# Optimization experiments

Hardware: AMD Instinct MI355X
Metric: run time of the kernel (lower is better)

## Reference

```python
import jax, jax.numpy as jnp
import numpy as np
import math

B, N, D = 4, 16384, 256
M, H = 64, 8
HD = D // H

def setup_inputs() -> dict:
    key = jax.random.key(0)
    ks = jax.random.split(key, 5)
    s = 1.0 / math.sqrt(D)
    return {
        "x": jax.random.normal(ks[0], (B, N, D), dtype=jnp.float32),
        "Ws": jax.random.normal(ks[1], (M, D), dtype=jnp.float32) * s,
        "bs": jnp.zeros((M,), dtype=jnp.float32),
        "Wqkv": jax.random.normal(ks[2], (3 * D, D), dtype=jnp.float32) * s,
        "Wo": jax.random.normal(ks[3], (D, D), dtype=jnp.float32) * s,
        "bo": jnp.zeros((D,), dtype=jnp.float32),
    }

def reference(x, Ws, bs, Wqkv, Wo, bo):
    # slice weights: softmax over N (dim=1), matching the torch code exactly
    logits = jnp.einsum('bnd,md->bnm', x, Ws) + bs          # [B,N,M]
    weights = jax.nn.softmax(logits, axis=1)                # softmax over N
    # pooling: tokens[b,m,d] = sum_n w[b,n,m] * x[b,n,d]
    tokens = jnp.einsum('bnm,bnd->bmd', weights, x)         # [B,M,D]
    # qkv projection (no bias)
    qkv = jnp.einsum('bmd,ed->bme', tokens, Wqkv)           # [B,M,3D]
    qkv = qkv.reshape(B, M, 3, H, HD)
    q = qkv[:, :, 0].transpose(0, 2, 1, 3)                  # [B,H,M,HD]
    k = qkv[:, :, 1].transpose(0, 2, 1, 3)
    v = qkv[:, :, 2].transpose(0, 2, 1, 3)
    scale = 1.0 / math.sqrt(HD)
    attn = jax.nn.softmax(jnp.einsum('bhmd,bhkd->bhmk', q, k) * scale, axis=-1)
    token_out = jnp.einsum('bhmk,bhkd->bhmd', attn, v)      # [B,H,M,HD]
    token_out = token_out.transpose(0, 2, 1, 3).reshape(B, M, D)
    token_out = jnp.einsum('bmd,ed->bme', token_out, Wo) + bo
    # unpooling: out[b,n,d] = sum_m w[b,n,m] * token_out[b,m,d]
    out = jnp.einsum('bnm,bmd->bnd', weights, token_out)    # [B,N,D]
    return out
```

## Files before the change

kernel.cpp:

```cpp
#include <hip/hip_runtime.h>
#include <math.h>

constexpr int B = 4;
constexpr int N = 16384;
constexpr int D = 256;
constexpr int M = 64;
constexpr int H = 8;

typedef __attribute__((ext_vector_type(8))) short short8;
typedef __attribute__((ext_vector_type(4))) float floatx4;

__device__ __forceinline__ float4 ld4(const float* p) {
  return *reinterpret_cast<const float4*>(p);
}
__device__ __forceinline__ unsigned short f2bf(float f) {
  unsigned u = __float_as_uint(f);
  unsigned r = (u + 0x7fffu + ((u >> 16) & 1u)) >> 16;
  return (unsigned short)r;
}

__global__ __launch_bounds__(256) void k0_prep(
    const float* __restrict__ Ws, const float* __restrict__ Wqkv,
    const float* __restrict__ Wo, unsigned short* __restrict__ WsB,
    unsigned short* __restrict__ WqkvB, unsigned short* __restrict__ WoB,
    float* __restrict__ denom, float* __restrict__ tokens,
    float* __restrict__ tokO) {
  const int g = blockIdx.x * 256 + threadIdx.x;
  if (g < 32768) {
    *reinterpret_cast<float2*>(&tokens[g * 2]) = make_float2(0.f, 0.f);
    *reinterpret_cast<float2*>(&tokO[g * 2]) = make_float2(0.f, 0.f);
  }
  if (g < 128)
    *reinterpret_cast<float2*>(&denom[g * 2]) = make_float2(0.f, 0.f);
  const float* src;
  unsigned short* dst;
  int off;
  if (g < 2048) {
    src = Ws; dst = WsB; off = g;
  } else if (g < 26624) {
    src = Wqkv; dst = WqkvB; off = g - 2048;
  } else {
    src = Wo; dst = WoB; off = g - 26624;
  }
  const float4 a = ld4(&src[(size_t)off * 8]);
  const float4 c = ld4(&src[(size_t)off * 8 + 4]);
  unsigned d0 = (unsigned)f2bf(a.x) | ((unsigned)f2bf(a.y) << 16);
  unsigned d1 = (unsigned)f2bf(a.z) | ((unsigned)f2bf(a.w) << 16);
  unsigned d2 = (unsigned)f2bf(c.x) | ((unsigned)f2bf(c.y) << 16);
  unsigned d3 = (unsigned)f2bf(c.z) | ((unsigned)f2bf(c.w) << 16);
  *reinterpret_cast<uint4*>(&dst[(size_t)off * 8]) = make_uint4(d0, d1, d2, d3);
}

__global__ __launch_bounds__(512, 4) void k1_fused(
    const float* __restrict__ x, const unsigned short* __restrict__ WsB,
    const float* __restrict__ bs, unsigned short* __restrict__ En,
    float* __restrict__ denom) {
  __shared__ unsigned short Wt[64][264];
  __shared__ float red[64];
  const int b = blockIdx.y;
  const int n0 = blockIdx.x * 128;
  const int tid = threadIdx.x;
  const int w = tid >> 6, l = tid & 63;
  const int l15 = l & 15;
  const int q8 = (l >> 4) * 8;
  const int ar = w * 16 + l15;

  float4 fx[16];
  const float* xrow = &x[((size_t)(b * N + n0 + ar)) * D];
#pragma unroll
  for (int ks = 0; ks < 8; ++ks) {
    fx[2 * ks] = ld4(&xrow[ks * 32 + q8]);
    fx[2 * ks + 1] = ld4(&xrow[ks * 32 + q8 + 4]);
  }
#pragma unroll
  for (int p = 0; p < 4; ++p) {
    const int u = p * 512 + tid;
    const int row = u >> 5;
    const int c = (u & 31) * 8;
    *reinterpret_cast<short8*>(&Wt[row][c]) =
        *reinterpret_cast<const short8*>(&WsB[(size_t)row * 256 + c]);
  }
  if (tid < 64) red[tid] = 0.0f;

  short8 afr[8];
#pragma unroll
  for (int ks = 0; ks < 8; ++ks) {
    const float4 a0 = fx[2 * ks], a1 = fx[2 * ks + 1];
    short8 t;
    t[0] = (short)f2bf(a0.x); t[1] = (short)f2bf(a0.y);
    t[2] = (short)f2bf(a0.z); t[3] = (short)f2bf(a0.w);
    t[4] = (short)f2bf(a1.x); t[5] = (short)f2bf(a1.y);
    t[6] = (short)f2bf(a1.z); t[7] = (short)f2bf(a1.w);
    afr[ks] = t;
  }
  __syncthreads();

  floatx4 acc[4] = {{0.f, 0.f, 0.f, 0.f},
                    {0.f, 0.f, 0.f, 0.f},
                    {0.f, 0.f, 0.f, 0.f},
                    {0.f, 0.f, 0.f, 0.f}};
#pragma unroll
  for (int ks = 0; ks < 8; ++ks) {
#pragma unroll
    for (int mt = 0; mt < 4; ++mt) {
      short8 bf = *reinterpret_cast<short8*>(&Wt[mt * 16 + l15][ks * 32 + q8]);
      acc[mt] = __builtin_amdgcn_mfma_f32_16x16x32_bf16(afr[ks], bf, acc[mt], 0, 0, 0);
    }
  }

#pragma unroll
  for (int mt = 0; mt < 4; ++mt) {
    const int m = mt * 16 + l15;
    const float bsm = bs[m];
    float s = 0.0f;
#pragma unroll
    for (int r = 0; r < 4; ++r) {
      const int n = w * 16 + (l >> 4) * 4 + r;
      const float e = expf(acc[mt][r] + bsm);
      s += e;
      En[((size_t)(b * N + n0 + n)) * M + m] = f2bf(e);
    }
    atomicAdd(&red[m], s);
  }
  __syncthreads();
  if (tid < 64) atomicAdd(&denom[b * M + tid], red[tid]);
}

__global__ __launch_bounds__(256) void k2_pool(
    const unsigned short* __restrict__ En, const float* __restrict__ x,
    float* __restrict__ tokens) {
  __shared__ unsigned short Ens[64][70];
  __shared__ unsigned short XsT[64][72];
  const int dt = blockIdx.x, nc = blockIdx.y, b = blockIdx.z;
  const int d0 = dt * 64;
  const int tid = threadIdx.x;
  const int w = tid >> 6, l = tid & 63;
  const int l15 = l & 15;
  const int q8 = (l >> 4) * 8;
  floatx4 acc[4] = {{0.f, 0.f, 0.f, 0.f},
                    {0.f, 0.f, 0.f, 0.f},
                    {0.f, 0.f, 0.f, 0.f},
                    {0.f, 0.f, 0.f, 0.f}};
  for (int kc = 0; kc < 4; ++kc) {
    const int nb = nc * 256 + kc * 64;
    __syncthreads();
#pragma unroll
    for (int p = 0; p < 2; ++p) {
      const int u = p * 256 + tid;
      const int n = u >> 3;
      const int c8 = (u & 7) * 8;
      short8 v = *reinterpret_cast<const short8*>(
          &En[((size_t)(b * N + nb + n)) * M + c8]);
      uint4 uv = *reinterpret_cast<uint4*>(&v);
      unsigned* dp = reinterpret_cast<unsigned*>(&Ens[n][c8]);
      dp[0] = uv.x; dp[1] = uv.y; dp[2] = uv.z; dp[3] = uv.w;
    }
    {
      const int n = tid >> 2;
      const int c16 = (tid & 3) * 16;
      const float* xp = &x[((size_t)(b * N + nb + n)) * D + d0 + c16];
#pragma unroll
      for (int q = 0; q < 4; ++q) {
        float4 v = ld4(xp + q * 4);
        XsT[c16 + q * 4 + 0][n] = f2bf(v.x);
        XsT[c16 + q * 4 + 1][n] = f2bf(v.y);
        XsT[c16 + q * 4 + 2][n] = f2bf(v.z);
        XsT[c16 + q * 4 + 3][n] = f2bf(v.w);
      }
    }
    __syncthreads();
#pragma unroll
    for (int ks = 0; ks < 2; ++ks) {
      const int nf = ks * 32 + q8;
      short8 a;
#pragma unroll
      for (int j = 0; j < 8; ++j) a[j] = (short)Ens[nf + j][w * 16 + l15];
#pragma unroll
      for (int dtile = 0; dtile < 4; ++dtile) {
        short8 bf = *reinterpret_cast<short8*>(&XsT[dtile * 16 + l15][nf]);
        acc[dtile] =
            __builtin_amdgcn_mfma_f32_16x16x32_bf16(a, bf, acc[dtile], 0, 0, 0);
      }
    }
  }
#pragma unroll
  for (int dtile = 0; dtile < 4; ++dtile)
#pragma unroll
    for (int r = 0; r < 4; ++r) {
      const int m = w * 16 + (l >> 4) * 4 + r;
      const int d = d0 + dtile * 16 + (l & 15);
      atomicAdd(&tokens[((size_t)(b * M + m)) * D + d], acc[dtile][r]);
    }
}

__global__ __launch_bounds__(256) void k_fa(
    const float* __restrict__ tokens, const unsigned short* __restrict__ WqkvB,
    const unsigned short* __restrict__ WoB, const float* __restrict__ denom,
    float* __restrict__ tokO) {
  __shared__ __align__(16) char smem[84480];
  unsigned short* const At = reinterpret_cast<unsigned short*>(smem);
  unsigned short* const Wq = reinterpret_cast<unsigned short*>(smem + 33792);
  float* const qt = reinterpret_cast<float*>(smem);
  float* const kt = reinterpret_cast<float*>(smem + 8704);
  float* const vv = reinterpret_cast<float*>(smem + 17408);
  float* const P  = reinterpret_cast<float*>(smem + 26624);
  float* const ao = reinterpret_cast<float*>(smem + 44032);
  const int b = blockIdx.x >> 3;
  const int h = blockIdx.x & 7;
  const int tid = threadIdx.x;
  const int w = tid >> 6, l = tid & 63;
  const int l15 = l & 15;
  const int q8 = (l >> 4) * 8;
  const int r4 = (l >> 4) * 4;

#pragma unroll
  for (int p = 0; p < 16; ++p) {
    const int i = p * 256 + tid;
    const int row = i >> 6;
    const int c4 = (i & 63) * 4;
    float4 av = ld4(&tokens[((size_t)(b * M + row)) * D + c4]);
    unsigned a0 = (unsigned)f2bf(av.x) | ((unsigned)f2bf(av.y) << 16);
    unsigned a1 = (unsigned)f2bf(av.z) | ((unsigned)f2bf(av.w) << 16);
    *reinterpret_cast<uint2*>(&At[row * 264 + c4]) = make_uint2(a0, a1);
  }
#pragma unroll
  for (int p = 0; p < 12; ++p) {
    const int u = p * 256 + tid;
    const int row = u >> 5;
    const int c = (u & 31) * 8;
    const int eg = (row < 32) ? (h * 32 + row)
                 : (row < 64) ? (256 + h * 32 + row - 32)
                              : (512 + h * 32 + row - 64);
    *reinterpret_cast<short8*>(&Wq[row * 264 + c]) =
        *reinterpret_cast<const short8*>(&WqkvB[(size_t)eg * 256 + c]);
  }
  float rcp4[4];
#pragma unroll
  for (int r = 0; r < 4; ++r)
    rcp4[r] = 1.0f / denom[b * M + w * 16 + r4 + r];
  __syncthreads();

  floatx4 acc[6] = {{0.f, 0.f, 0.f, 0.f}, {0.f, 0.f, 0.f, 0.f},
                    {0.f, 0.f, 0.f, 0.f}, {0.f, 0.f, 0.f, 0.f},
                    {0.f, 0.f, 0.f, 0.f}, {0.f, 0.f, 0.f, 0.f}};
  const int arow = w * 16 + l15;
#pragma unroll
  for (int ks = 0; ks < 8; ++ks) {
    short8 a = *reinterpret_cast<short8*>(&At[arow * 264 + ks * 32 + q8]);
#pragma unroll
    for (int et = 0; et < 6; ++et) {
      short8 bf = *reinterpret_cast<short8*>(&Wq[(et * 16 + l15) * 264 + ks * 32 + q8]);
      acc[et] = __builtin_amdgcn_mfma_f32_16x16x32_bf16(a, bf, acc[et], 0, 0, 0);
    }
  }
  short8 wof[4];
#pragma unroll
  for (int dt4 = 0; dt4 < 4; ++dt4)
    wof[dt4] = *reinterpret_cast<const short8*>(
        &WoB[(size_t)(w * 64 + dt4 * 16 + l15) * 256 + h * 32 + q8]);
  __syncthreads();

#pragma unroll
  for (int r = 0; r < 4; ++r) {
    const int m = w * 16 + r4 + r;
    const float rc = rcp4[r];
#pragma unroll
    for (int et = 0; et < 6; ++et) {
      const float val = acc[et][r] * rc;
      const int c = (et & 1) * 16 + l15;
      if (et < 2) qt[c * 68 + m] = val;
      else if (et < 4) kt[c * 68 + m] = val;
      else vv[m * 36 + c] = val;
    }
  }
  __syncthreads();

  {
    const int tm4 = (tid & 15) * 4;
    const int tn4 = (tid >> 4) * 4;
    float sacc[4][4] = {};
    for (int k = 0; k < 32; ++k) {
      float4 a4 = ld4(&qt[k * 68 + tn4]);
      float4 b4 = ld4(&kt[k * 68 + tm4]);
#pragma unroll
      for (int i = 0; i < 4; ++i) {
        const float av = (i == 0) ? a4.x : (i == 1) ? a4.y : (i == 2) ? a4.z : a4.w;
        sacc[i][0] = fmaf(av, b4.x, sacc[i][0]);
        sacc[i][1] = fmaf(av, b4.y, sacc[i][1]);
        sacc[i][2] = fmaf(av, b4.z, sacc[i][2]);
        sacc[i][3] = fmaf(av, b4.w, sacc[i][3]);
      }
    }
    const float scale = 0.17677669529663687f;
#pragma unroll
    for (int i = 0; i < 4; ++i)
      *reinterpret_cast<float4*>(&P[(tn4 + i) * 68 + tm4]) =
          make_float4(sacc[i][0] * scale, sacc[i][1] * scale,
                      sacc[i][2] * scale, sacc[i][3] * scale);
  }
  __syncthreads();
  if (tid < 64) {
    float mx = -1e30f;
    for (int j = 0; j < 64; ++j) mx = fmaxf(mx, P[tid * 68 + j]);
    float s = 0.0f;
    for (int j = 0; j < 64; ++j) {
      const float e = expf(P[tid * 68 + j] - mx);
      P[tid * 68 + j] = e;
      s += e;
    }
    const float r = 1.0f / s;
    for (int j = 0; j < 64; ++j) P[tid * 68 + j] *= r;
  }
  __syncthreads();
  if (tid < 128) {
    const int i0 = (tid >> 3) * 4;
    const int c0 = (tid & 7) * 4;
    float o[4][4] = {};
    for (int j = 0; j < 64; ++j) {
      float4 v4 = ld4(&vv[j * 36 + c0]);
#pragma unroll
      for (int ii = 0; ii < 4; ++ii) {
        const float p = P[(i0 + ii) * 68 + j];
        o[ii][0] = fmaf(p, v4.x, o[ii][0]);
        o[ii][1] = fmaf(p, v4.y, o[ii][1]);
        o[ii][2] = fmaf(p, v4.z, o[ii][2]);
        o[ii][3] = fmaf(p, v4.w, o[ii][3]);
      }
    }
#pragma unroll
    for (int ii = 0; ii < 4; ++ii)
#pragma unroll
      for (int jj = 0; jj < 4; ++jj) ao[(i0 + ii) * 36 + c0 + jj] = o[ii][jj];
  }
  __syncthreads();

  floatx4 acc2[4][4] = {{{0.f, 0.f, 0.f, 0.f}, {0.f, 0.f, 0.f, 0.f},
                         {0.f, 0.f, 0.f, 0.f}, {0.f, 0.f, 0.f, 0.f}},
                        {{0.f, 0.f, 0.f, 0.f}, {0.f, 0.f, 0.f, 0.f},
                         {0.f, 0.f, 0.f, 0.f}, {0.f, 0.f, 0.f, 0.f}},
                        {{0.f, 0.f, 0.f, 0.f}, {0.f, 0.f, 0.f, 0.f},
                         {0.f, 0.f, 0.f, 0.f}, {0.f, 0.f, 0.f, 0.f}},
                        {{0.f, 0.f, 0.f, 0.f}, {0.f, 0.f, 0.f, 0.f},
                         {0.f, 0.f, 0.f, 0.f}, {0.f, 0.f, 0.f, 0.f}}};
#pragma unroll
  for (int mt = 0; mt < 4; ++mt) {
    short8 af;
#pragma unroll
    for (int j = 0; j < 8; ++j)
      af[j] = (short)f2bf(ao[(mt * 16 + l15) * 36 + q8 + j]);
#pragma unroll
    for (int dt4 = 0; dt4 < 4; ++dt4)
      acc2[mt][dt4] =
          __builtin_amdgcn_mfma_f32_16x16x32_bf16(af, wof[dt4], acc2[mt][dt4], 0, 0, 0);
  }
#pragma unroll
  for (int mt = 0; mt < 4; ++mt)
#pragma unroll
    for (int dt4 = 0; dt4 < 4; ++dt4)
#pragma unroll
      for (int r = 0; r < 4; ++r) {
        const int m = mt * 16 + r4 + r;
        const int d = w * 64 + dt4 * 16 + l15;
        atomicAdd(&tokO[((size_t)(b * M + m)) * D + d], acc2[mt][dt4][r]);
      }
}

__global__ __launch_bounds__(512, 4) void k6_unpool(
    const unsigned short* __restrict__ En, const float* __restrict__ tokO,
    const float* __restrict__ denom, const float* __restrict__ bo,
    float* __restrict__ out) {
  __shared__ unsigned short EnS[128][72];
  __shared__ unsigned short TpS[64][72];
  const int dt = blockIdx.x, nt = blockIdx.y, b = blockIdx.z;
  const int n0 = nt * 128, d0 = dt * 64;
  const int tid = threadIdx.x;
  const int w = tid >> 6, l = tid & 63;
  const int l15 = l & 15;
  const int q8 = (l >> 4) * 8;
#pragma unroll
  for (int p = 0; p < 2; ++p) {
    const int g = p * 512 + tid;
    const int row = g >> 3;
    const int c8 = (g & 7) * 8;
    *reinterpret_cast<short8*>(&EnS[row][c8]) =
        *reinterpret_cast<const short8*>(
            &En[((size_t)(b * N + n0 + row)) * M + c8]);
  }
  {
    const int m = tid >> 3;
    const int c8 = (tid & 7) * 8;
    const float rc = 1.0f / denom[b * M + m];
    const float* tp = &tokO[((size_t)(b * M + m)) * D + d0 + c8];
    float4 v0 = ld4(tp);
    float4 v1 = ld4(tp + 4);
    float4 bb0 = ld4(&bo[d0 + c8]);
    float4 bb1 = ld4(&bo[d0 + c8 + 4]);
    TpS[c8 + 0][m] = f2bf((v0.x + bb0.x) * rc);
    TpS[c8 + 1][m] = f2bf((v0.y + bb0.y) * rc);
    TpS[c8 + 2][m] = f2bf((v0.z + bb0.z) * rc);
    TpS[c8 + 3][m] = f2bf((v0.w + bb0.w) * rc);
    TpS[c8 + 4][m] = f2bf((v1.x + bb1.x) * rc);
    TpS[c8 + 5][m] = f2bf((v1.y + bb1.y) * rc);
    TpS[c8 + 6][m] = f2bf((v1.z + bb1.z) * rc);
    TpS[c8 + 7][m] = f2bf((v1.w + bb1.w) * rc);
  }
  __syncthreads();
  floatx4 acc[4] = {{0.f, 0.f, 0.f, 0.f},
                    {0.f, 0.f, 0.f, 0.f},
                    {0.f, 0.f, 0.f, 0.f},
                    {0.f, 0.f, 0.f, 0.f}};
  const int arow = w * 16 + l15;
#pragma unroll
  for (int ks = 0; ks < 2; ++ks) {
    short8 a = *reinterpret_cast<short8*>(&EnS[arow][ks * 32 + q8]);
#pragma unroll
    for (int dtile = 0; dtile < 4; ++dtile) {
      short8 bf = *reinterpret_cast<short8*>(
          &TpS[dtile * 16 + l15][ks * 32 + q8]);
      acc[dtile] =
          __builtin_amdgcn_mfma_f32_16x16x32_bf16(a, bf, acc[dtile], 0, 0, 0);
    }
  }
#pragma unroll
  for (int dtile = 0; dtile < 4; ++dtile)
#pragma unroll
    for (int r = 0; r < 4; ++r) {
      const int n = n0 + w * 16 + (l >> 4) * 4 + r;
      const int d = d0 + dtile * 16 + l15;
      out[((size_t)(b * N + n)) * D + d] = acc[dtile][r];
    }
}

extern "C" void kernel_launch(void* const* d_in, const int* in_sizes, int n_in,
                              void* d_out, int out_size, void* d_ws,
                              size_t ws_size, hipStream_t stream) {
  const float* x = (const float*)d_in[0];
  const float* Ws = (const float*)d_in[1];
  const float* bs = (const float*)d_in[2];
  const float* Wqkv = (const float*)d_in[3];
  const float* Wo = (const float*)d_in[4];
  const float* bo = (const float*)d_in[5];
  float* out = (float*)d_out;

  char* p = (char*)d_ws;
  unsigned short* En = (unsigned short*)p;    p += (size_t)B * N * M * 2;
  float* denom = (float*)p;                   p += (size_t)B * M * 4;
  float* tokens = (float*)p;                  p += (size_t)B * M * D * 4;
  float* tokO = (float*)p;                    p += (size_t)B * M * D * 4;
  unsigned short* WsB = (unsigned short*)p;   p += (size_t)M * D * 2;
  unsigned short* WqkvB = (unsigned short*)p; p += (size_t)3 * D * D * 2;
  unsigned short* WoB = (unsigned short*)p;   p += (size_t)D * D * 2;

  k0_prep<<<dim3(136), 256, 0, stream>>>(Ws, Wqkv, Wo, WsB, WqkvB, WoB,
                                         denom, tokens, tokO);
  k1_fused<<<dim3(N / 128, B), 512, 0, stream>>>(x, WsB, bs, En, denom);
  k2_pool<<<dim3(D / 64, N / 256, B), 256, 0, stream>>>(En, x, tokens);
  k_fa<<<dim3(B * H), 256, 0, stream>>>(tokens, WqkvB, WoB, denom, tokO);
  k6_unpool<<<dim3(D / 64, N / 128, B), 512, 0, stream>>>(En, tokO, denom, bo,
                                                          out);
}
```

Measured before the change: 174.6 us.

## Fuse slice-logit exp kernel with pooling GEMM to reuse x tile on-chip

Merges the logit/exp kernel and the pooling kernel into one. Each block now processes 128 tokens in two 64-row passes, keeping the bf16 x fragments and the exp weights in shared memory and feeding them straight into the pooling MFMAs. This removes the second full read of x and the En read-back in the pool kernel, plus one launch. In exchange, per-block register pressure rises (16 accumulator tiles), blocks shrink to 256 threads, and each block now issues 64x256 atomic adds to tokens, so global atomic traffic grows.

```diff
diff --git a/kernel.cpp b/kernel.cpp
--- a/kernel.cpp
+++ b/kernel.cpp
@@ -51,145 +51,125 @@
   *reinterpret_cast<uint4*>(&dst[(size_t)off * 8]) = make_uint4(d0, d1, d2, d3);
 }
 
-__global__ __launch_bounds__(512, 4) void k1_fused(
+__global__ __launch_bounds__(256, 2) void k12_fused(
     const float* __restrict__ x, const unsigned short* __restrict__ WsB,
     const float* __restrict__ bs, unsigned short* __restrict__ En,
-    float* __restrict__ denom) {
+    float* __restrict__ denom, float* __restrict__ tokens) {
   __shared__ unsigned short Wt[64][264];
+  __shared__ unsigned short EsT[64][70];
+  __shared__ unsigned short XsT[256][70];
   __shared__ float red[64];
   const int b = blockIdx.y;
-  const int n0 = blockIdx.x * 128;
+  const int nb0 = blockIdx.x * 128;
   const int tid = threadIdx.x;
   const int w = tid >> 6, l = tid & 63;
   const int l15 = l & 15;
   const int q8 = (l >> 4) * 8;
+  const int r4 = (l >> 4) * 4;
   const int ar = w * 16 + l15;
 
-  float4 fx[16];
-  const float* xrow = &x[((size_t)(b * N + n0 + ar)) * D];
-#pragma unroll
-  for (int ks = 0; ks < 8; ++ks) {
-    fx[2 * ks] = ld4(&xrow[ks * 32 + q8]);
-    fx[2 * ks + 1] = ld4(&xrow[ks * 32 + q8 + 4]);
-  }
-#pragma unroll
-  for (int p = 0; p < 4; ++p) {
-    const int u = p * 512 + tid;
+#pragma unroll
+  for (int p = 0; p < 8; ++p) {
+    const int u = p * 256 + tid;
     const int row = u >> 5;
     const int c = (u & 31) * 8;
     *reinterpret_cast<short8*>(&Wt[row][c]) =
         *reinterpret_cast<const short8*>(&WsB[(size_t)row * 256 + c]);
   }
   if (tid < 64) red[tid] = 0.0f;
-
-  short8 afr[8];
-#pragma unroll
-  for (int ks = 0; ks < 8; ++ks) {
-    const float4 a0 = fx[2 * ks], a1 = fx[2 * ks + 1];
-    short8 t;
-    t[0] = (short)f2bf(a0.x); t[1] = (short)f2bf(a0.y);
-    t[2] = (short)f2bf(a0.z); t[3] = (short)f2bf(a0.w);
-    t[4] = (short)f2bf(a1.x); t[5] = (short)f2bf(a1.y);
-    t[6] = (short)f2bf(a1.z); t[7] = (short)f2bf(a1.w);
-    afr[ks] = t;
-  }
-  __syncthreads();
-
-  floatx4 acc[4] = {{0.f, 0.f, 0.f, 0.f},
-                    {0.f, 0.f, 0.f, 0.f},
-                    {0.f, 0.f, 0.f, 0.f},
-                    {0.f, 0.f, 0.f, 0.f}};
-#pragma unroll
-  for (int ks = 0; ks < 8; ++ks) {
+  __syncthreads();
+
+  floatx4 acc2[16];
+#pragma unroll
+  for (int i = 0; i < 16; ++i) acc2[i] = {0.f, 0.f, 0.f, 0.f};
+
+  for (int t = 0; t < 2; ++t) {
+    const int n0 = nb0 + t * 64;
+    float4 fx[16];
+    const float* xrow = &x[((size_t)(b * N + n0 + ar)) * D];
+#pragma unroll
+    for (int ks = 0; ks < 8; ++ks) {
+      fx[2 * ks] = ld4(&xrow[ks * 32 + q8]);
+      fx[2 * ks + 1] = ld4(&xrow[ks * 32 + q8 + 4]);
+    }
+    short8 afr[8];
+#pragma unroll
+    for (int ks = 0; ks < 8; ++ks) {
+      const float4 a0 = fx[2 * ks], a1 = fx[2 * ks + 1];
+      short8 tt;
+      tt[0] = (short)f2bf(a0.x); tt[1] = (short)f2bf(a0.y);
+      tt[2] = (short)f2bf(a0.z); tt[3] = (short)f2bf(a0.w);
+      tt[4] = (short)f2bf(a1.x); tt[5] = (short)f2bf(a1.y);
+      tt[6] = (short)f2bf(a1.z); tt[7] = (short)f2bf(a1.w);
+      afr[ks] = tt;
+    }
+
+    floatx4 acc[4] = {{0.f, 0.f, 0.f, 0.f},
+                      {0.f, 0.f, 0.f, 0.f},
+                      {0.f, 0.f, 0.f, 0.f},
+                      {0.f, 0.f, 0.f, 0.f}};
+#pragma unroll
+    for (int ks = 0; ks < 8; ++ks) {
+#pragma unroll
+      for (int mt = 0; mt < 4; ++mt) {
+        short8 bf = *reinterpret_cast<short8*>(&Wt[mt * 16 + l15][ks * 32 + q8]);
+        acc[mt] =
+            __builtin_amdgcn_mfma_f32_16x16x32_bf16(afr[ks], bf, acc[mt], 0, 0, 0);
+      }
+    }
+
+    unsigned short ebf[16];
 #pragma unroll
     for (int mt = 0; mt < 4; ++mt) {
-      short8 bf = *reinterpret_cast<short8*>(&Wt[mt * 16 + l15][ks * 32 + q8]);
-      acc[mt] = __builtin_amdgcn_mfma_f32_16x16x32_bf16(afr[ks], bf, acc[mt], 0, 0, 0);
-    }
-  }
-
-#pragma unroll
-  for (int mt = 0; mt < 4; ++mt) {
-    const int m = mt * 16 + l15;
-    const float bsm = bs[m];
-    float s = 0.0f;
-#pragma unroll
-    for (int r = 0; r < 4; ++r) {
-      const int n = w * 16 + (l >> 4) * 4 + r;
-      const float e = expf(acc[mt][r] + bsm);
-      s += e;
-      En[((size_t)(b * N + n0 + n)) * M + m] = f2bf(e);
-    }
-    atomicAdd(&red[m], s);
-  }
-  __syncthreads();
-  if (tid < 64) atomicAdd(&denom[b * M + tid], red[tid]);
-}
-
-__global__ __launch_bounds__(256) void k2_pool(
-    const unsigned short* __restrict__ En, const float* __restrict__ x,
-    float* __restrict__ tokens) {
-  __shared__ unsigned short Ens[64][70];
-  __shared__ unsigned short XsT[64][72];
-  const int dt = blockIdx.x, nc = blockIdx.y, b = blockIdx.z;
-  const int d0 = dt * 64;
-  const int tid = threadIdx.x;
-  const int w = tid >> 6, l = tid & 63;
-  const int l15 = l & 15;
-  const int q8 = (l >> 4) * 8;
-  floatx4 acc[4] = {{0.f, 0.f, 0.f, 0.f},
-                    {0.f, 0.f, 0.f, 0.f},
-                    {0.f, 0.f, 0.f, 0.f},
-                    {0.f, 0.f, 0.f, 0.f}};
-  for (int kc = 0; kc < 4; ++kc) {
-    const int nb = nc * 256 + kc * 64;
+      const int m = mt * 16 + l15;
+      const float bsm = bs[m];
+      float s = 0.0f;
+#pragma unroll
+      for (int r = 0; r < 4; ++r) {
+        const int n = w * 16 + r4 + r;
+        const float e = expf(acc[mt][r] + bsm);
+        s += e;
+        const unsigned short eb = f2bf(e);
+        ebf[mt * 4 + r] = eb;
+        En[((size_t)(b * N + n0 + n)) * M + m] = eb;
+      }
+      atomicAdd(&red[m], s);
+    }
+
     __syncthreads();
 #pragma unroll
-    for (int p = 0; p < 2; ++p) {
-      const int u = p * 256 + tid;
-      const int n = u >> 3;
-      const int c8 = (u & 7) * 8;
-      short8 v = *reinterpret_cast<const short8*>(
-          &En[((size_t)(b * N + nb + n)) * M + c8]);
-      uint4 uv = *reinterpret_cast<uint4*>(&v);
-      unsigned* dp = reinterpret_cast<unsigned*>(&Ens[n][c8]);
-      dp[0] = uv.x; dp[1] = uv.y; dp[2] = uv.z; dp[3] = uv.w;
-    }
-    {
-      const int n = tid >> 2;
-      const int c16 = (tid & 3) * 16;
-      const float* xp = &x[((size_t)(b * N + nb + n)) * D + d0 + c16];
-#pragma unroll
-      for (int q = 0; q < 4; ++q) {
-        float4 v = ld4(xp + q * 4);
-        XsT[c16 + q * 4 + 0][n] = f2bf(v.x);
-        XsT[c16 + q * 4 + 1][n] = f2bf(v.y);
-        XsT[c16 + q * 4 + 2][n] = f2bf(v.z);
-        XsT[c16 + q * 4 + 3][n] = f2bf(v.w);
-      }
-    }
+    for (int ks = 0; ks < 8; ++ks)
+#pragma unroll
+      for (int j = 0; j < 8; ++j)
+        XsT[ks * 32 + q8 + j][ar] = (unsigned short)afr[ks][j];
+#pragma unroll
+    for (int mt = 0; mt < 4; ++mt)
+#pragma unroll
+      for (int r = 0; r < 4; ++r)
+        EsT[mt * 16 + l15][w * 16 + r4 + r] = ebf[mt * 4 + r];
     __syncthreads();
+
 #pragma unroll
     for (int ks = 0; ks < 2; ++ks) {
       const int nf = ks * 32 + q8;
-      short8 a;
-#pragma unroll
-      for (int j = 0; j < 8; ++j) a[j] = (short)Ens[nf + j][w * 16 + l15];
-#pragma unroll
-      for (int dtile = 0; dtile < 4; ++dtile) {
-        short8 bf = *reinterpret_cast<short8*>(&XsT[dtile * 16 + l15][nf]);
-        acc[dtile] =
-            __builtin_amdgcn_mfma_f32_16x16x32_bf16(a, bf, acc[dtile], 0, 0, 0);
-      }
-    }
-  }
-#pragma unroll
-  for (int dtile = 0; dtile < 4; ++dtile)
+      short8 a = *reinterpret_cast<short8*>(&EsT[w * 16 + l15][nf]);
+#pragma unroll
+      for (int dt4 = 0; dt4 < 16; ++dt4) {
+        short8 bf = *reinterpret_cast<short8*>(&XsT[dt4 * 16 + l15][nf]);
+        acc2[dt4] =
+            __builtin_amdgcn_mfma_f32_16x16x32_bf16(a, bf, acc2[dt4], 0, 0, 0);
+      }
+    }
+  }
+
+  if (tid < 64) atomicAdd(&denom[b * M + tid], red[tid]);
+#pragma unroll
+  for (int dt4 = 0; dt4 < 16; ++dt4)
 #pragma unroll
     for (int r = 0; r < 4; ++r) {
-      const int m = w * 16 + (l >> 4) * 4 + r;
-      const int d = d0 + dtile * 16 + (l & 15);
-      atomicAdd(&tokens[((size_t)(b * M + m)) * D + d], acc[dtile][r]);
+      const int m = w * 16 + r4 + r;
+      const int d = dt4 * 16 + l15;
+      atomicAdd(&tokens[((size_t)(b * M + m)) * D + d], acc2[dt4][r]);
     }
 }
 
@@ -453,8 +433,8 @@
 
   k0_prep<<<dim3(136), 256, 0, stream>>>(Ws, Wqkv, Wo, WsB, WqkvB, WoB,
                                          denom, tokens, tokO);
-  k1_fused<<<dim3(N / 128, B), 512, 0, stream>>>(x, WsB, bs, En, denom);
-  k2_pool<<<dim3(D / 64, N / 256, B), 256, 0, stream>>>(En, x, tokens);
+  k12_fused<<<dim3(N / 128, B), 256, 0, stream>>>(x, WsB, bs, En, denom,
+                                                  tokens);
   k_fa<<<dim3(B * H), 256, 0, stream>>>(tokens, WqkvB, WoB, denom, tokO);
   k6_unpool<<<dim3(D / 64, N / 128, B), 512, 0, stream>>>(En, tokO, denom, bo,
                                                           out);
```

New measurement: 176.3 us. Within noise of the previous version (+1.0%).

## Replace global atomics with per-slot partials and a reduce kernel; drop prep kernel

Applied to the files above, without the earlier changes.

Pooling and denominator accumulation now write per-chunk partial sums to workspace slots. A new reduce kernel sums them, zeroes tokO, converts tokens to bf16 and precomputes reciprocal denominators. This removes float atomics and the separate prep/zero kernel. Weight conversion to bf16 moves inline into the consuming kernels, expf becomes __expf, and unpool blocks cover 256 rows in two passes. The cost is extra global traffic for the partial buffers (about 16 MB written then read) plus one more launch.

```diff
diff --git a/kernel.cpp b/kernel.cpp
--- a/kernel.cpp
+++ b/kernel.cpp
@@ -6,6 +6,8 @@
 constexpr int D = 256;
 constexpr int M = 64;
 constexpr int H = 8;
+constexpr int NSLOT_T = 64;
+constexpr int NSLOT_D = 128;
 
 typedef __attribute__((ext_vector_type(8))) short short8;
 typedef __attribute__((ext_vector_type(4))) float floatx4;
@@ -18,43 +20,18 @@
   unsigned r = (u + 0x7fffu + ((u >> 16) & 1u)) >> 16;
   return (unsigned short)r;
 }
-
-__global__ __launch_bounds__(256) void k0_prep(
-    const float* __restrict__ Ws, const float* __restrict__ Wqkv,
-    const float* __restrict__ Wo, unsigned short* __restrict__ WsB,
-    unsigned short* __restrict__ WqkvB, unsigned short* __restrict__ WoB,
-    float* __restrict__ denom, float* __restrict__ tokens,
-    float* __restrict__ tokO) {
-  const int g = blockIdx.x * 256 + threadIdx.x;
-  if (g < 32768) {
-    *reinterpret_cast<float2*>(&tokens[g * 2]) = make_float2(0.f, 0.f);
-    *reinterpret_cast<float2*>(&tokO[g * 2]) = make_float2(0.f, 0.f);
-  }
-  if (g < 128)
-    *reinterpret_cast<float2*>(&denom[g * 2]) = make_float2(0.f, 0.f);
-  const float* src;
-  unsigned short* dst;
-  int off;
-  if (g < 2048) {
-    src = Ws; dst = WsB; off = g;
-  } else if (g < 26624) {
-    src = Wqkv; dst = WqkvB; off = g - 2048;
-  } else {
-    src = Wo; dst = WoB; off = g - 26624;
-  }
-  const float4 a = ld4(&src[(size_t)off * 8]);
-  const float4 c = ld4(&src[(size_t)off * 8 + 4]);
+__device__ __forceinline__ uint2 pack8(float4 a, float4 b, unsigned* hi) {
   unsigned d0 = (unsigned)f2bf(a.x) | ((unsigned)f2bf(a.y) << 16);
   unsigned d1 = (unsigned)f2bf(a.z) | ((unsigned)f2bf(a.w) << 16);
-  unsigned d2 = (unsigned)f2bf(c.x) | ((unsigned)f2bf(c.y) << 16);
-  unsigned d3 = (unsigned)f2bf(c.z) | ((unsigned)f2bf(c.w) << 16);
-  *reinterpret_cast<uint4*>(&dst[(size_t)off * 8]) = make_uint4(d0, d1, d2, d3);
-}
-
-__global__ __launch_bounds__(512, 4) void k1_fused(
-    const float* __restrict__ x, const unsigned short* __restrict__ WsB,
+  hi[0] = (unsigned)f2bf(b.x) | ((unsigned)f2bf(b.y) << 16);
+  hi[1] = (unsigned)f2bf(b.z) | ((unsigned)f2bf(b.w) << 16);
+  return make_uint2(d0, d1);
+}
+
+__global__ __launch_bounds__(512, 4) void k1_logits(
+    const float* __restrict__ x, const float* __restrict__ Ws,
     const float* __restrict__ bs, unsigned short* __restrict__ En,
-    float* __restrict__ denom) {
+    float* __restrict__ denomP) {
   __shared__ unsigned short Wt[64][264];
   __shared__ float red[64];
   const int b = blockIdx.y;
@@ -63,6 +40,7 @@
   const int w = tid >> 6, l = tid & 63;
   const int l15 = l & 15;
   const int q8 = (l >> 4) * 8;
+  const int r4 = (l >> 4) * 4;
   const int ar = w * 16 + l15;
 
   float4 fx[16];
@@ -73,12 +51,17 @@
     fx[2 * ks + 1] = ld4(&xrow[ks * 32 + q8 + 4]);
   }
 #pragma unroll
-  for (int p = 0; p < 4; ++p) {
-    const int u = p * 512 + tid;
-    const int row = u >> 5;
-    const int c = (u & 31) * 8;
-    *reinterpret_cast<short8*>(&Wt[row][c]) =
-        *reinterpret_cast<const short8*>(&WsB[(size_t)row * 256 + c]);
+  for (int p = 0; p < 2; ++p) {
+    const int i = p * 512 + tid;
+    const int row = i >> 4;
+    const int c16 = (i & 15) * 16;
+    const float* wp = &Ws[(size_t)row * 256 + c16];
+    float4 v0 = ld4(wp), v1 = ld4(wp + 4), v2 = ld4(wp + 8), v3 = ld4(wp + 12);
+    unsigned hi[2];
+    uint2 lo = pack8(v0, v1, hi);
+    *reinterpret_cast<uint4*>(&Wt[row][c16]) = make_uint4(lo.x, lo.y, hi[0], hi[1]);
+    lo = pack8(v2, v3, hi);
+    *reinterpret_cast<uint4*>(&Wt[row][c16 + 8]) = make_uint4(lo.x, lo.y, hi[0], hi[1]);
   }
   if (tid < 64) red[tid] = 0.0f;
 
@@ -115,20 +98,21 @@
     float s = 0.0f;
 #pragma unroll
     for (int r = 0; r < 4; ++r) {
-      const int n = w * 16 + (l >> 4) * 4 + r;
-      const float e = expf(acc[mt][r] + bsm);
+      const int n = w * 16 + r4 + r;
+      const float e = __expf(acc[mt][r] + bsm);
       s += e;
       En[((size_t)(b * N + n0 + n)) * M + m] = f2bf(e);
     }
     atomicAdd(&red[m], s);
   }
   __syncthreads();
-  if (tid < 64) atomicAdd(&denom[b * M + tid], red[tid]);
+  if (tid < 64)
+    denomP[((size_t)(b * NSLOT_D) + blockIdx.x) * M + tid] = red[tid];
 }
 
 __global__ __launch_bounds__(256) void k2_pool(
     const unsigned short* __restrict__ En, const float* __restrict__ x,
-    float* __restrict__ tokens) {
+    float* __restrict__ tokensP) {
   __shared__ unsigned short Ens[64][70];
   __shared__ unsigned short XsT[64][72];
   const int dt = blockIdx.x, nc = blockIdx.y, b = blockIdx.z;
@@ -183,19 +167,46 @@
       }
     }
   }
+  float* op = tokensP + ((size_t)(b * NSLOT_T + nc) * M) * D;
 #pragma unroll
   for (int dtile = 0; dtile < 4; ++dtile)
 #pragma unroll
     for (int r = 0; r < 4; ++r) {
       const int m = w * 16 + (l >> 4) * 4 + r;
-      const int d = d0 + dtile * 16 + (l & 15);
-      atomicAdd(&tokens[((size_t)(b * M + m)) * D + d], acc[dtile][r]);
-    }
+      op[(size_t)m * D + d0 + dtile * 16 + l15] = acc[dtile][r];
+    }
+}
+
+__global__ __launch_bounds__(256) void k2r_reduce(
+    const float* __restrict__ tokensP, const float* __restrict__ denomP,
+    unsigned short* __restrict__ tokensB, float* __restrict__ rdenom,
+    float* __restrict__ tokO) {
+  const int b = blockIdx.x >> 6;
+  const int m = blockIdx.x & 63;
+  const int d = threadIdx.x;
+  tokO[(size_t)blockIdx.x * 256 + d] = 0.0f;
+  const float* base = tokensP + ((size_t)(b * NSLOT_T) * M + m) * D + d;
+  float s0 = 0.f, s1 = 0.f, s2 = 0.f, s3 = 0.f;
+#pragma unroll 4
+  for (int s = 0; s < NSLOT_T; s += 4) {
+    s0 += base[(size_t)(s + 0) * M * D];
+    s1 += base[(size_t)(s + 1) * M * D];
+    s2 += base[(size_t)(s + 2) * M * D];
+    s3 += base[(size_t)(s + 3) * M * D];
+  }
+  tokensB[((size_t)(b * M) + m) * D + d] = f2bf((s0 + s1) + (s2 + s3));
+  if (d < 64) {
+    float v = denomP[((size_t)(b * NSLOT_D) + d) * M + m] +
+              denomP[((size_t)(b * NSLOT_D) + 64 + d) * M + m];
+#pragma unroll
+    for (int off = 32; off > 0; off >>= 1) v += __shfl_down(v, off);
+    if (d == 0) rdenom[b * M + m] = 1.0f / v;
+  }
 }
 
 __global__ __launch_bounds__(256) void k_fa(
-    const float* __restrict__ tokens, const unsigned short* __restrict__ WqkvB,
-    const unsigned short* __restrict__ WoB, const float* __restrict__ denom,
+    const unsigned short* __restrict__ tokensB, const float* __restrict__ Wqkv,
+    const float* __restrict__ Wo, const float* __restrict__ rdenom,
     float* __restrict__ tokO) {
   __shared__ __align__(16) char smem[84480];
   unsigned short* const At = reinterpret_cast<unsigned short*>(smem);
@@ -214,30 +225,35 @@
   const int r4 = (l >> 4) * 4;
 
 #pragma unroll
-  for (int p = 0; p < 16; ++p) {
-    const int i = p * 256 + tid;
-    const int row = i >> 6;
-    const int c4 = (i & 63) * 4;
-    float4 av = ld4(&tokens[((size_t)(b * M + row)) * D + c4]);
-    unsigned a0 = (unsigned)f2bf(av.x) | ((unsigned)f2bf(av.y) << 16);
-    unsigned a1 = (unsigned)f2bf(av.z) | ((unsigned)f2bf(av.w) << 16);
-    *reinterpret_cast<uint2*>(&At[row * 264 + c4]) = make_uint2(a0, a1);
-  }
-#pragma unroll
-  for (int p = 0; p < 12; ++p) {
+  for (int p = 0; p < 8; ++p) {
     const int u = p * 256 + tid;
     const int row = u >> 5;
     const int c = (u & 31) * 8;
+    *reinterpret_cast<short8*>(&At[row * 264 + c]) =
+        *reinterpret_cast<const short8*>(&tokensB[((size_t)(b * M + row)) * 256 + c]);
+  }
+#pragma unroll
+  for (int p = 0; p < 6; ++p) {
+    const int u = p * 256 + tid;
+    const int row = u >> 4;
+    const int c16 = (u & 15) * 16;
     const int eg = (row < 32) ? (h * 32 + row)
                  : (row < 64) ? (256 + h * 32 + row - 32)
                               : (512 + h * 32 + row - 64);
-    *reinterpret_cast<short8*>(&Wq[row * 264 + c]) =
-        *reinterpret_cast<const short8*>(&WqkvB[(size_t)eg * 256 + c]);
+    const float* wp = &Wqkv[(size_t)eg * 256 + c16];
+    float4 v0 = ld4(wp), v1 = ld4(wp + 4), v2 = ld4(wp + 8), v3 = ld4(wp + 12);
+    unsigned hi[2];
+    uint2 lo = pack8(v0, v1, hi);
+    *reinterpret_cast<uint4*>(&Wq[row * 264 + c16]) =
+        make_uint4(lo.x, lo.y, hi[0], hi[1]);
+    lo = pack8(v2, v3, hi);
+    *reinterpret_cast<uint4*>(&Wq[row * 264 + c16 + 8]) =
+        make_uint4(lo.x, lo.y, hi[0], hi[1]);
   }
   float rcp4[4];
 #pragma unroll
   for (int r = 0; r < 4; ++r)
-    rcp4[r] = 1.0f / denom[b * M + w * 16 + r4 + r];
+    rcp4[r] = rdenom[b * M + w * 16 + r4 + r];
   __syncthreads();
 
   floatx4 acc[6] = {{0.f, 0.f, 0.f, 0.f}, {0.f, 0.f, 0.f, 0.f},
@@ -255,9 +271,16 @@
   }
   short8 wof[4];
 #pragma unroll
-  for (int dt4 = 0; dt4 < 4; ++dt4)
-    wof[dt4] = *reinterpret_cast<const short8*>(
-        &WoB[(size_t)(w * 64 + dt4 * 16 + l15) * 256 + h * 32 + q8]);
+  for (int dt4 = 0; dt4 < 4; ++dt4) {
+    const float* wp = &Wo[(size_t)(w * 64 + dt4 * 16 + l15) * 256 + h * 32 + q8];
+    float4 v0 = ld4(wp), v1 = ld4(wp + 4);
+    short8 tt;
+    tt[0] = (short)f2bf(v0.x); tt[1] = (short)f2bf(v0.y);
+    tt[2] = (short)f2bf(v0.z); tt[3] = (short)f2bf(v0.w);
+    tt[4] = (short)f2bf(v1.x); tt[5] = (short)f2bf(v1.y);
+    tt[6] = (short)f2bf(v1.z); tt[7] = (short)f2bf(v1.w);
+    wof[dt4] = tt;
+  }
   __syncthreads();
 
 #pragma unroll
@@ -367,18 +390,18 @@
 
 __global__ __launch_bounds__(512, 4) void k6_unpool(
     const unsigned short* __restrict__ En, const float* __restrict__ tokO,
-    const float* __restrict__ denom, const float* __restrict__ bo,
+    const float* __restrict__ rdenom, const float* __restrict__ bo,
     float* __restrict__ out) {
-  __shared__ unsigned short EnS[128][72];
+  __shared__ unsigned short EnS[256][72];
   __shared__ unsigned short TpS[64][72];
   const int dt = blockIdx.x, nt = blockIdx.y, b = blockIdx.z;
-  const int n0 = nt * 128, d0 = dt * 64;
+  const int n0 = nt * 256, d0 = dt * 64;
   const int tid = threadIdx.x;
   const int w = tid >> 6, l = tid & 63;
   const int l15 = l & 15;
   const int q8 = (l >> 4) * 8;
 #pragma unroll
-  for (int p = 0; p < 2; ++p) {
+  for (int p = 0; p < 4; ++p) {
     const int g = p * 512 + tid;
     const int row = g >> 3;
     const int c8 = (g & 7) * 8;
@@ -389,7 +412,7 @@
   {
     const int m = tid >> 3;
     const int c8 = (tid & 7) * 8;
-    const float rc = 1.0f / denom[b * M + m];
+    const float rc = rdenom[b * M + m];
     const float* tp = &tokO[((size_t)(b * M + m)) * D + d0 + c8];
     float4 v0 = ld4(tp);
     float4 v1 = ld4(tp + 4);
@@ -405,30 +428,33 @@
     TpS[c8 + 7][m] = f2bf((v1.w + bb1.w) * rc);
   }
   __syncthreads();
-  floatx4 acc[4] = {{0.f, 0.f, 0.f, 0.f},
-                    {0.f, 0.f, 0.f, 0.f},
-                    {0.f, 0.f, 0.f, 0.f},
-                    {0.f, 0.f, 0.f, 0.f}};
-  const int arow = w * 16 + l15;
-#pragma unroll
-  for (int ks = 0; ks < 2; ++ks) {
-    short8 a = *reinterpret_cast<short8*>(&EnS[arow][ks * 32 + q8]);
-#pragma unroll
-    for (int dtile = 0; dtile < 4; ++dtile) {
-      short8 bf = *reinterpret_cast<short8*>(
-          &TpS[dtile * 16 + l15][ks * 32 + q8]);
-      acc[dtile] =
-          __builtin_amdgcn_mfma_f32_16x16x32_bf16(a, bf, acc[dtile], 0, 0, 0);
-    }
-  }
-#pragma unroll
-  for (int dtile = 0; dtile < 4; ++dtile)
-#pragma unroll
-    for (int r = 0; r < 4; ++r) {
-      const int n = n0 + w * 16 + (l >> 4) * 4 + r;
-      const int d = d0 + dtile * 16 + l15;
-      out[((size_t)(b * N + n)) * D + d] = acc[dtile][r];
-    }
+#pragma unroll
+  for (int pass = 0; pass < 2; ++pass) {
+    const int arow = pass * 128 + w * 16 + l15;
+    floatx4 acc[4] = {{0.f, 0.f, 0.f, 0.f},
+                      {0.f, 0.f, 0.f, 0.f},
+                      {0.f, 0.f, 0.f, 0.f},
+                      {0.f, 0.f, 0.f, 0.f}};
+#pragma unroll
+    for (int ks = 0; ks < 2; ++ks) {
+      short8 a = *reinterpret_cast<short8*>(&EnS[arow][ks * 32 + q8]);
+#pragma unroll
+      for (int dtile = 0; dtile < 4; ++dtile) {
+        short8 bf = *reinterpret_cast<short8*>(
+            &TpS[dtile * 16 + l15][ks * 32 + q8]);
+        acc[dtile] =
+            __builtin_amdgcn_mfma_f32_16x16x32_bf16(a, bf, acc[dtile], 0, 0, 0);
+      }
+    }
+#pragma unroll
+    for (int dtile = 0; dtile < 4; ++dtile)
+#pragma unroll
+      for (int r = 0; r < 4; ++r) {
+        const int n = n0 + pass * 128 + w * 16 + (l >> 4) * 4 + r;
+        const int d = d0 + dtile * 16 + l15;
+        out[((size_t)(b * N + n)) * D + d] = acc[dtile][r];
+      }
+  }
 }
 
 extern "C" void kernel_launch(void* const* d_in, const int* in_sizes, int n_in,
@@ -443,19 +469,18 @@
   float* out = (float*)d_out;
 
   char* p = (char*)d_ws;
-  unsigned short* En = (unsigned short*)p;    p += (size_t)B * N * M * 2;
-  float* denom = (float*)p;                   p += (size_t)B * M * 4;
-  float* tokens = (float*)p;                  p += (size_t)B * M * D * 4;
-  float* tokO = (float*)p;                    p += (size_t)B * M * D * 4;
-  unsigned short* WsB = (unsigned short*)p;   p += (size_t)M * D * 2;
-  unsigned short* WqkvB = (unsigned short*)p; p += (size_t)3 * D * D * 2;
-  unsigned short* WoB = (unsigned short*)p;   p += (size_t)D * D * 2;
-
-  k0_prep<<<dim3(136), 256, 0, stream>>>(Ws, Wqkv, Wo, WsB, WqkvB, WoB,
-                                         denom, tokens, tokO);
-  k1_fused<<<dim3(N / 128, B), 512, 0, stream>>>(x, WsB, bs, En, denom);
-  k2_pool<<<dim3(D / 64, N / 256, B), 256, 0, stream>>>(En, x, tokens);
-  k_fa<<<dim3(B * H), 256, 0, stream>>>(tokens, WqkvB, WoB, denom, tokO);
-  k6_unpool<<<dim3(D / 64, N / 128, B), 512, 0, stream>>>(En, tokO, denom, bo,
+  unsigned short* En = (unsigned short*)p;  p += (size_t)B * N * M * 2;
+  float* tokensP = (float*)p;               p += (size_t)B * NSLOT_T * M * D * 4;
+  float* denomP = (float*)p;                p += (size_t)B * NSLOT_D * M * 4;
+  float* rdenom = (float*)p;                p += (size_t)B * M * 4;
+  unsigned short* tokensB = (unsigned short*)p; p += (size_t)B * M * D * 2;
+  float* tokO = (float*)p;                  p += (size_t)B * M * D * 4;
+
+  k1_logits<<<dim3(N / 128, B), 512, 0, stream>>>(x, Ws, bs, En, denomP);
+  k2_pool<<<dim3(D / 64, N / 256, B), 256, 0, stream>>>(En, x, tokensP);
+  k2r_reduce<<<dim3(B * M), 256, 0, stream>>>(tokensP, denomP, tokensB,
+                                              rdenom, tokO);
+  k_fa<<<dim3(B * H), 256, 0, stream>>>(tokensB, Wqkv, Wo, rdenom, tokO);
+  k6_unpool<<<dim3(D / 64, N / 256, B), 512, 0, stream>>>(En, tokO, rdenom, bo,
                                                           out);
 }
```

After: 173.9 us. About the same (-0.4%).
